# Kernel optimization log

Hardware: AMD Instinct MI355X
Metric: run time of the kernel (lower is better)

The kernel has to match this reference:

```python
import jax, jax.numpy as jnp
import numpy as np
from jax import lax

D_MODEL = 1024
STATE_DIM = 32
GROUPS = 8
GROUP_DIM = D_MODEL // GROUPS
DT_MIN = 0.001
DT_MAX = 0.1
EPS = 1e-6


def setup_inputs() -> dict:
    key = jax.random.key(0)
    ks = jax.random.split(key, 6)
    B, T = 4, 4096
    u = jax.random.normal(ks[0], (B, T, D_MODEL), dtype=jnp.float32)
    state = jnp.zeros((B, GROUPS, STATE_DIM), dtype=jnp.float32)
    A_log = jax.random.normal(ks[1], (GROUPS, STATE_DIM), dtype=jnp.float32) * 0.02
    B_param = jax.random.normal(ks[2], (GROUPS, STATE_DIM, GROUP_DIM), dtype=jnp.float32) * 0.02
    C = jax.random.normal(ks[3], (GROUPS, GROUP_DIM, STATE_DIM), dtype=jnp.float32) * 0.02
    Dp = jnp.zeros((GROUPS, GROUP_DIM), dtype=jnp.float32)
    dt_logit = jnp.zeros((GROUPS,), dtype=jnp.float32)
    return {"u": u, "state": state, "A_log": A_log, "B_param": B_param,
            "C": C, "Dp": Dp, "dt_logit": dt_logit}


def reference(u, state, A_log, B_param, C, Dp, dt_logit):
    Bsz, T, Dm = u.shape
    A = -jax.nn.softplus(A_log)                                  # [G,N]
    dt = DT_MIN + (DT_MAX - DT_MIN) * jax.nn.sigmoid(dt_logit)   # [G]
    dt_g = dt[:, None]                                           # [G,1]
    Abar = jnp.exp(A * dt_g)                                     # [G,N]
    # (exp(A dt) - 1)/A, stable for small |A|
    frac = jnp.where(jnp.abs(A) > EPS, (Abar - 1.0) / A,
                     jnp.broadcast_to(dt_g, A.shape))            # [G,N]
    Bbar = frac[..., None] * B_param                             # [G,N,gd]

    u_g = u.reshape(Bsz, T, GROUPS, GROUP_DIM)                   # [B,T,G,gd]
    # precompute input injections for all timesteps, then scan the LTI recurrence
    Bu = jnp.einsum('btgi,gni->btgn', u_g, Bbar)                 # [B,T,G,N]
    Bu_t = jnp.moveaxis(Bu, 1, 0)                                # [T,B,G,N]

    def step(s, bu):
        s = s * Abar + bu                                        # [B,G,N]
        return s, s

    s_final, states = lax.scan(step, state, Bu_t)                # states: [T,B,G,N]
    Cs = jnp.einsum('tbgn,gdn->btgd', states, C)                 # [B,T,G,gd]
    y = (Cs + Dp * u_g).reshape(Bsz, T, Dm)                      # [B,T,D]
    return y, s_final
```

## Files before the change

### kernel.cpp

```cpp
#include <hip/hip_runtime.h>
#include <hip/hip_bf16.h>

#define DM 1024
#define SD 32
#define NG 8
#define GD 128
#define BS 4
#define TT 4096
#define CL 64
#define NC (TT/CL)

typedef __attribute__((ext_vector_type(8))) short short8;
typedef __attribute__((ext_vector_type(4))) float f32x4;

#define WS_POWA  0
#define WS_STL   65536
#define WS_CARRY (WS_STL + 8388608)
#define WS_PAL   (WS_CARRY + 262144)

__device__ __forceinline__ unsigned short f2bf(float f) {
  __hip_bfloat16 h = __float2bfloat16(f);
  return __builtin_bit_cast(unsigned short, h);
}
__device__ __forceinline__ float bf2f(unsigned short h) {
  return __uint_as_float(((unsigned)h) << 16);
}
__device__ __forceinline__ float softplus_f(float x) {
  return (x > 20.f) ? x : log1pf(expf(x));
}
__device__ __forceinline__ short8 pack8(float4 a, float4 b) {
  short8 h;
  h[0]=(short)f2bf(a.x); h[1]=(short)f2bf(a.y); h[2]=(short)f2bf(a.z); h[3]=(short)f2bf(a.w);
  h[4]=(short)f2bf(b.x); h[5]=(short)f2bf(b.y); h[6]=(short)f2bf(b.z); h[7]=(short)f2bf(b.w);
  return h;
}

__global__ __launch_bounds__(64) void ka_bu_scan(const float* __restrict__ u,
                                                 const float* __restrict__ A_log,
                                                 const float* __restrict__ B_param,
                                                 const float* __restrict__ dt_logit,
                                                 unsigned char* __restrict__ ws) {
  const int bx = blockIdx.x;
  const int c = bx & (NC - 1);
  const int g = (bx >> 6) & (NG - 1);
  const int b = bx >> 9;
  const int l = threadIdx.x;
  const int lr = l & 15, lh = l >> 4;

  const float dtg = 0.001f + 0.099f * (1.f / (1.f + expf(-dt_logit[g])));

  float fracv[2];
  #pragma unroll
  for (int nt = 0; nt < 2; ++nt) {
    int n = nt * 16 + lr;
    float A = -softplus_f(A_log[g * SD + n]);
    float a = expf(A * dtg);
    fracv[nt] = (fabsf(A) > 1e-6f) ? (a - 1.f) / A : dtg;
  }
  float a_scan;
  {
    float A = -softplus_f(A_log[g * SD + (l & 31)]);
    a_scan = expf(A * dtg);
  }

  const float* bp = B_param + (size_t)g * SD * GD;
  short8 bfr[4][2];
  #pragma unroll
  for (int kt = 0; kt < 4; ++kt)
    #pragma unroll
    for (int nt = 0; nt < 2; ++nt) {
      const float* p = bp + (size_t)(nt * 16 + lr) * GD + kt * 32 + lh * 8;
      float4 v0 = *(const float4*)p;
      float4 v1 = *(const float4*)(p + 4);
      float s = fracv[nt];
      v0.x*=s; v0.y*=s; v0.z*=s; v0.w*=s;
      v1.x*=s; v1.y*=s; v1.z*=s; v1.w*=s;
      bfr[kt][nt] = pack8(v0, v1);
    }

  const float* up = u + ((size_t)b * TT + (size_t)c * CL) * DM + g * GD;
  float4 ub[2][4][2];
  #pragma unroll
  for (int kt = 0; kt < 2; ++kt)
    #pragma unroll
    for (int m = 0; m < 4; ++m) {
      const float* p = up + (size_t)(m * 16 + lr) * DM + kt * 32 + lh * 8;
      ub[kt][m][0] = *(const float4*)p;
      ub[kt][m][1] = *(const float4*)(p + 4);
    }

  f32x4 acc[4][2];
  #pragma unroll
  for (int m = 0; m < 4; ++m)
    #pragma unroll
    for (int nt = 0; nt < 2; ++nt)
      #pragma unroll
      for (int j = 0; j < 4; ++j) acc[m][nt][j] = 0.f;

  #pragma unroll
  for (int kt = 0; kt < 4; ++kt) {
    short8 af[4];
    #pragma unroll
    for (int m = 0; m < 4; ++m)
      af[m] = pack8(ub[kt & 1][m][0], ub[kt & 1][m][1]);
    if (kt < 2) {
      #pragma unroll
      for (int m = 0; m < 4; ++m) {
        const float* p = up + (size_t)(m * 16 + lr) * DM + (kt + 2) * 32 + lh * 8;
        ub[kt & 1][m][0] = *(const float4*)p;
        ub[kt & 1][m][1] = *(const float4*)(p + 4);
      }
    }
    #pragma unroll
    for (int m = 0; m < 4; ++m)
      #pragma unroll
      for (int nt = 0; nt < 2; ++nt)
        acc[m][nt] = __builtin_amdgcn_mfma_f32_16x16x32_bf16(af[m], bfr[kt][nt], acc[m][nt], 0, 0, 0);
  }

  __shared__ __align__(16) float sBu[CL * 33];
  __shared__ __align__(16) unsigned short sSt[CL * SD];
  #pragma unroll
  for (int m = 0; m < 4; ++m)
    #pragma unroll
    for (int nt = 0; nt < 2; ++nt)
      #pragma unroll
      for (int j = 0; j < 4; ++j) {
        int t = m * 16 + lh * 4 + j;
        sBu[t * 33 + (nt * 16 + lr)] = acc[m][nt][j];
      }
  __syncthreads();

  float* carry = (float*)(ws + WS_CARRY);
  if (l < SD) {
    float s = 0.f;
    #pragma unroll
    for (int t = 0; t < CL; ++t) {
      s = fmaf(s, a_scan, sBu[t * 33 + l]);
      sSt[t * SD + l] = f2bf(s);
    }
    carry[((b * NG + g) * NC + c) * SD + l] = s;
  }
  __syncthreads();

  unsigned short* stg = (unsigned short*)(ws + WS_STL) + ((size_t)((b * NC + c) * NG + g)) * CL * SD;
  #pragma unroll
  for (int p = 0; p < 4; ++p) {
    int off = (p * 64 + l) * 8;
    *(short8*)(stg + off) = *(short8*)(sSt + off);
  }

  if (b == 0 && c == 0 && l < SD) {
    float* powA = (float*)(ws + WS_POWA);
    float* powAL = (float*)(ws + WS_PAL);
    float p = 1.f;
    #pragma unroll
    for (int t = 0; t < CL; ++t) {
      p *= a_scan;
      powA[(g * CL + t) * SD + l] = p;
    }
    float aL = p;
    float q = 1.f;
    #pragma unroll
    for (int j = 0; j < CL; ++j) {
      powAL[(g * CL + j) * SD + l] = q;
      q *= aL;
    }
  }
}

__global__ __launch_bounds__(128) void kb_y(const float* __restrict__ u,
                                            const float* __restrict__ state0,
                                            const float* __restrict__ C,
                                            const float* __restrict__ Dp,
                                            unsigned char* __restrict__ ws,
                                            float* __restrict__ y,
                                            float* __restrict__ sfin) {
  const int bx = blockIdx.x;
  const int c = bx & (NC - 1);
  const int g = (bx >> 6) & (NG - 1);
  const int b = bx >> 9;
  const int tid = threadIdx.x;
  const int w = tid >> 6;
  const int l = tid & 63;
  const int lr = l & 15, lh = l >> 4;
  const int n = l & 31;

  const float* powA = (const float*)(ws + WS_POWA) + g * CL * SD;
  const float* powAL = (const float*)(ws + WS_PAL) + g * CL * SD;
  const float* carry = (const float*)(ws + WS_CARRY) + (size_t)(b * NG + g) * NC * SD;
  const unsigned short* stg = (const unsigned short*)(ws + WS_STL) + ((size_t)((b * NC + c) * NG + g)) * CL * SD;

  __shared__ __align__(16) float sY[32 * 132];

  bool need_u;
  {
    float2 dpc = *(const float2*)(Dp + g * GD + l * 2);
    need_u = __ballot((dpc.x != 0.f) || (dpc.y != 0.f)) != 0ULL;
  }

  float p;
  {
    float a0 = 0.f, a1 = 0.f, a2 = 0.f, a3 = 0.f;
    int cc = 0;
    while (cc + 8 <= c) {
      float ca[8], wt[8];
      #pragma unroll
      for (int e = 0; e < 8; ++e) {
        ca[e] = carry[(cc + e) * SD + n];
        wt[e] = powAL[(c - 1 - cc - e) * SD + n];
      }
      a0 = fmaf(wt[0], ca[0], a0); a1 = fmaf(wt[1], ca[1], a1);
      a2 = fmaf(wt[2], ca[2], a2); a3 = fmaf(wt[3], ca[3], a3);
      a0 = fmaf(wt[4], ca[4], a0); a1 = fmaf(wt[5], ca[5], a1);
      a2 = fmaf(wt[6], ca[6], a2); a3 = fmaf(wt[7], ca[7], a3);
      cc += 8;
    }
    for (; cc < c; ++cc)
      a0 = fmaf(powAL[(c - 1 - cc) * SD + n], carry[cc * SD + n], a0);
    p = fmaf(state0[(b * NG + g) * SD + n], powAL[c * SD + n], (a0 + a1) + (a2 + a3));
  }
  if (w == 0 && c == NC - 1 && l < SD) {
    const float aL = powA[(CL - 1) * SD + l];
    sfin[(b * NG + g) * SD + l] = fmaf(p, aL, carry[(NC - 1) * SD + l]);
  }

  float pr[8];
  #pragma unroll
  for (int e = 0; e < 8; ++e) pr[e] = __shfl(p, lh * 8 + e);

  short8 sf[4];
  #pragma unroll
  for (int tt = 0; tt < 4; ++tt) {
    int t = tt * 16 + lr;
    short8 sl = *(const short8*)(stg + t * SD + lh * 8);
    const float* pw = powA + t * SD + lh * 8;
    float4 pw0 = *(const float4*)pw;
    float4 pw1 = *(const float4*)(pw + 4);
    short8 hh;
    hh[0] = (short)f2bf(bf2f((unsigned short)sl[0]) + pw0.x * pr[0]);
    hh[1] = (short)f2bf(bf2f((unsigned short)sl[1]) + pw0.y * pr[1]);
    hh[2] = (short)f2bf(bf2f((unsigned short)sl[2]) + pw0.z * pr[2]);
    hh[3] = (short)f2bf(bf2f((unsigned short)sl[3]) + pw0.w * pr[3]);
    hh[4] = (short)f2bf(bf2f((unsigned short)sl[4]) + pw1.x * pr[4]);
    hh[5] = (short)f2bf(bf2f((unsigned short)sl[5]) + pw1.y * pr[5]);
    hh[6] = (short)f2bf(bf2f((unsigned short)sl[6]) + pw1.z * pr[6]);
    hh[7] = (short)f2bf(bf2f((unsigned short)sl[7]) + pw1.w * pr[7]);
    sf[tt] = hh;
  }

  const float* cp = C + (size_t)g * GD * SD;
  const size_t rowbase = ((size_t)b * TT + (size_t)c * CL) * DM + g * GD;

  short8 cf[4];
  #pragma unroll
  for (int dd = 0; dd < 4; ++dd) {
    int d = (w * 4 + dd) * 16 + lr;
    const float* pp = cp + (size_t)d * SD + lh * 8;
    float4 v0 = *(const float4*)pp;
    float4 v1 = *(const float4*)(pp + 4);
    cf[dd] = pack8(v0, v1);
  }
  f32x4 acc[4][4];
  #pragma unroll
  for (int dd = 0; dd < 4; ++dd)
    #pragma unroll
    for (int tt = 0; tt < 4; ++tt) {
      f32x4 z;
      #pragma unroll
      for (int j = 0; j < 4; ++j) z[j] = 0.f;
      acc[dd][tt] = __builtin_amdgcn_mfma_f32_16x16x32_bf16(cf[dd], sf[tt], z, 0, 0, 0);
    }

  const int sd4 = (tid & 31) * 4;
  float4 dpv = *(const float4*)(Dp + g * GD + sd4);

  #pragma unroll
  for (int tp = 0; tp < 2; ++tp) {
    if (tp) __syncthreads();
    #pragma unroll
    for (int dd = 0; dd < 4; ++dd)
      #pragma unroll
      for (int q = 0; q < 2; ++q) {
        int tt = tp * 2 + q;
        int tl = q * 16 + lr;
        int d0 = (w * 4 + dd) * 16 + lh * 4;
        *(float4*)(sY + tl * 132 + d0) = (float4){acc[dd][tt][0], acc[dd][tt][1],
                                                  acc[dd][tt][2], acc[dd][tt][3]};
      }
    __syncthreads();
    #pragma unroll
    for (int r = 0; r < 8; ++r) {
      int tl = r * 4 + (tid >> 5);
      int t = tp * 32 + tl;
      float4 v = *(const float4*)(sY + tl * 132 + sd4);
      size_t off = rowbase + (size_t)t * DM + sd4;
      if (need_u) {
        float4 u4 = *(const float4*)(u + off);
        v.x += dpv.x * u4.x; v.y += dpv.y * u4.y;
        v.z += dpv.z * u4.z; v.w += dpv.w * u4.w;
      }
      *(float4*)(y + off) = v;
    }
  }
}

extern "C" void kernel_launch(void* const* d_in, const int* in_sizes, int n_in,
                              void* d_out, int out_size, void* d_ws, size_t ws_size,
                              hipStream_t stream) {
  const float* u       = (const float*)d_in[0];
  const float* state0  = (const float*)d_in[1];
  const float* A_log   = (const float*)d_in[2];
  const float* B_param = (const float*)d_in[3];
  const float* C       = (const float*)d_in[4];
  const float* Dp      = (const float*)d_in[5];
  const float* dtl     = (const float*)d_in[6];
  float* y = (float*)d_out;
  unsigned char* ws = (unsigned char*)d_ws;
  float* sfin = y + (size_t)BS * TT * DM;

  ka_bu_scan<<<dim3(BS * NG * NC), dim3(64), 0, stream>>>(u, A_log, B_param, dtl, ws);
  kb_y<<<dim3(BS * NG * NC), dim3(128), 0, stream>>>(u, state0, C, Dp, ws, y, sfin);
}
```

Before: 43.44 us.

## Process two chunks per block in kb_y with 256 threads

The output kernel now handles two consecutive time chunks per block, using 4 waves that each own 2 d-tiles instead of 2 waves with 4. The carry-prefix reduction runs once for the first chunk, and the second chunk's prefix comes from one extra FMA. This removes half of the serial O(c) carry sums and halves the C fragment loads per chunk. In exchange there are half as many blocks and extra barriers between the two chunk passes that share the sY buffer.

```diff
diff --git a/kernel.cpp b/kernel.cpp
--- a/kernel.cpp
+++ b/kernel.cpp
@@ -169,66 +169,16 @@
   }
 }
 
-__global__ __launch_bounds__(128) void kb_y(const float* __restrict__ u,
-                                            const float* __restrict__ state0,
-                                            const float* __restrict__ C,
-                                            const float* __restrict__ Dp,
-                                            unsigned char* __restrict__ ws,
-                                            float* __restrict__ y,
-                                            float* __restrict__ sfin) {
-  const int bx = blockIdx.x;
-  const int c = bx & (NC - 1);
-  const int g = (bx >> 6) & (NG - 1);
-  const int b = bx >> 9;
-  const int tid = threadIdx.x;
-  const int w = tid >> 6;
-  const int l = tid & 63;
-  const int lr = l & 15, lh = l >> 4;
-  const int n = l & 31;
-
-  const float* powA = (const float*)(ws + WS_POWA) + g * CL * SD;
-  const float* powAL = (const float*)(ws + WS_PAL) + g * CL * SD;
-  const float* carry = (const float*)(ws + WS_CARRY) + (size_t)(b * NG + g) * NC * SD;
-  const unsigned short* stg = (const unsigned short*)(ws + WS_STL) + ((size_t)((b * NC + c) * NG + g)) * CL * SD;
-
-  __shared__ __align__(16) float sY[32 * 132];
-
-  bool need_u;
-  {
-    float2 dpc = *(const float2*)(Dp + g * GD + l * 2);
-    need_u = __ballot((dpc.x != 0.f) || (dpc.y != 0.f)) != 0ULL;
-  }
-
-  float p;
-  {
-    float a0 = 0.f, a1 = 0.f, a2 = 0.f, a3 = 0.f;
-    int cc = 0;
-    while (cc + 8 <= c) {
-      float ca[8], wt[8];
-      #pragma unroll
-      for (int e = 0; e < 8; ++e) {
-        ca[e] = carry[(cc + e) * SD + n];
-        wt[e] = powAL[(c - 1 - cc - e) * SD + n];
-      }
-      a0 = fmaf(wt[0], ca[0], a0); a1 = fmaf(wt[1], ca[1], a1);
-      a2 = fmaf(wt[2], ca[2], a2); a3 = fmaf(wt[3], ca[3], a3);
-      a0 = fmaf(wt[4], ca[4], a0); a1 = fmaf(wt[5], ca[5], a1);
-      a2 = fmaf(wt[6], ca[6], a2); a3 = fmaf(wt[7], ca[7], a3);
-      cc += 8;
-    }
-    for (; cc < c; ++cc)
-      a0 = fmaf(powAL[(c - 1 - cc) * SD + n], carry[cc * SD + n], a0);
-    p = fmaf(state0[(b * NG + g) * SD + n], powAL[c * SD + n], (a0 + a1) + (a2 + a3));
-  }
-  if (w == 0 && c == NC - 1 && l < SD) {
-    const float aL = powA[(CL - 1) * SD + l];
-    sfin[(b * NG + g) * SD + l] = fmaf(p, aL, carry[(NC - 1) * SD + l]);
-  }
-
-  float pr[8];
-  #pragma unroll
-  for (int e = 0; e < 8; ++e) pr[e] = __shfl(p, lh * 8 + e);
-
+__device__ __forceinline__ void kb_chunk(const unsigned short* __restrict__ stg,
+                                         const float* __restrict__ powA,
+                                         const float (&pr)[8],
+                                         const short8 (&cf)[2],
+                                         float* __restrict__ sY,
+                                         const float* __restrict__ u,
+                                         float* __restrict__ y,
+                                         size_t rowbase,
+                                         float4 dpv, bool need_u,
+                                         int tid, int w, int lr, int lh) {
   short8 sf[4];
   #pragma unroll
   for (int tt = 0; tt < 4; ++tt) {
@@ -249,21 +199,9 @@
     sf[tt] = hh;
   }
 
-  const float* cp = C + (size_t)g * GD * SD;
-  const size_t rowbase = ((size_t)b * TT + (size_t)c * CL) * DM + g * GD;
-
-  short8 cf[4];
-  #pragma unroll
-  for (int dd = 0; dd < 4; ++dd) {
-    int d = (w * 4 + dd) * 16 + lr;
-    const float* pp = cp + (size_t)d * SD + lh * 8;
-    float4 v0 = *(const float4*)pp;
-    float4 v1 = *(const float4*)(pp + 4);
-    cf[dd] = pack8(v0, v1);
-  }
-  f32x4 acc[4][4];
-  #pragma unroll
-  for (int dd = 0; dd < 4; ++dd)
+  f32x4 acc[2][4];
+  #pragma unroll
+  for (int dd = 0; dd < 2; ++dd)
     #pragma unroll
     for (int tt = 0; tt < 4; ++tt) {
       f32x4 z;
@@ -273,25 +211,23 @@
     }
 
   const int sd4 = (tid & 31) * 4;
-  float4 dpv = *(const float4*)(Dp + g * GD + sd4);
-
   #pragma unroll
   for (int tp = 0; tp < 2; ++tp) {
-    if (tp) __syncthreads();
-    #pragma unroll
-    for (int dd = 0; dd < 4; ++dd)
+    __syncthreads();
+    #pragma unroll
+    for (int dd = 0; dd < 2; ++dd)
       #pragma unroll
       for (int q = 0; q < 2; ++q) {
         int tt = tp * 2 + q;
         int tl = q * 16 + lr;
-        int d0 = (w * 4 + dd) * 16 + lh * 4;
+        int d0 = (w * 2 + dd) * 16 + lh * 4;
         *(float4*)(sY + tl * 132 + d0) = (float4){acc[dd][tt][0], acc[dd][tt][1],
                                                   acc[dd][tt][2], acc[dd][tt][3]};
       }
     __syncthreads();
     #pragma unroll
-    for (int r = 0; r < 8; ++r) {
-      int tl = r * 4 + (tid >> 5);
+    for (int r = 0; r < 4; ++r) {
+      int tl = r * 8 + (tid >> 5);
       int t = tp * 32 + tl;
       float4 v = *(const float4*)(sY + tl * 132 + sd4);
       size_t off = rowbase + (size_t)t * DM + sd4;
@@ -303,6 +239,90 @@
       *(float4*)(y + off) = v;
     }
   }
+}
+
+__global__ __launch_bounds__(256) void kb_y(const float* __restrict__ u,
+                                            const float* __restrict__ state0,
+                                            const float* __restrict__ C,
+                                            const float* __restrict__ Dp,
+                                            unsigned char* __restrict__ ws,
+                                            float* __restrict__ y,
+                                            float* __restrict__ sfin) {
+  const int bx = blockIdx.x;
+  const int pc = bx & (NC / 2 - 1);
+  const int g = (bx >> 5) & (NG - 1);
+  const int b = bx >> 8;
+  const int c0 = pc * 2;
+  const int tid = threadIdx.x;
+  const int w = tid >> 6;
+  const int l = tid & 63;
+  const int lr = l & 15, lh = l >> 4;
+  const int n = l & 31;
+
+  const float* powA = (const float*)(ws + WS_POWA) + g * CL * SD;
+  const float* powAL = (const float*)(ws + WS_PAL) + g * CL * SD;
+  const float* carry = (const float*)(ws + WS_CARRY) + (size_t)(b * NG + g) * NC * SD;
+  const unsigned short* stg0 = (const unsigned short*)(ws + WS_STL) + ((size_t)((b * NC + c0) * NG + g)) * CL * SD;
+  const unsigned short* stg1 = stg0 + (size_t)NG * CL * SD;
+
+  __shared__ __align__(16) float sY[32 * 132];
+
+  bool need_u;
+  {
+    float2 dpc = *(const float2*)(Dp + g * GD + l * 2);
+    need_u = __ballot((dpc.x != 0.f) || (dpc.y != 0.f)) != 0ULL;
+  }
+
+  float p0;
+  {
+    float a0 = 0.f, a1 = 0.f, a2 = 0.f, a3 = 0.f;
+    int cc = 0;
+    while (cc + 8 <= c0) {
+      float ca[8], wt[8];
+      #pragma unroll
+      for (int e = 0; e < 8; ++e) {
+        ca[e] = carry[(cc + e) * SD + n];
+        wt[e] = powAL[(c0 - 1 - cc - e) * SD + n];
+      }
+      a0 = fmaf(wt[0], ca[0], a0); a1 = fmaf(wt[1], ca[1], a1);
+      a2 = fmaf(wt[2], ca[2], a2); a3 = fmaf(wt[3], ca[3], a3);
+      a0 = fmaf(wt[4], ca[4], a0); a1 = fmaf(wt[5], ca[5], a1);
+      a2 = fmaf(wt[6], ca[6], a2); a3 = fmaf(wt[7], ca[7], a3);
+      cc += 8;
+    }
+    for (; cc < c0; ++cc)
+      a0 = fmaf(powAL[(c0 - 1 - cc) * SD + n], carry[cc * SD + n], a0);
+    p0 = fmaf(state0[(b * NG + g) * SD + n], powAL[c0 * SD + n], (a0 + a1) + (a2 + a3));
+  }
+  const float aL = powA[(CL - 1) * SD + n];
+  const float p1 = fmaf(p0, aL, carry[c0 * SD + n]);
+  if (pc == NC / 2 - 1 && w == 0 && l < SD)
+    sfin[(b * NG + g) * SD + l] = fmaf(p1, aL, carry[(NC - 1) * SD + l]);
+
+  float pr0[8], pr1[8];
+  #pragma unroll
+  for (int e = 0; e < 8; ++e) {
+    pr0[e] = __shfl(p0, lh * 8 + e);
+    pr1[e] = __shfl(p1, lh * 8 + e);
+  }
+
+  const float* cp = C + (size_t)g * GD * SD;
+  short8 cf[2];
+  #pragma unroll
+  for (int dd = 0; dd < 2; ++dd) {
+    int d = (w * 2 + dd) * 16 + lr;
+    const float* pp = cp + (size_t)d * SD + lh * 8;
+    float4 v0 = *(const float4*)pp;
+    float4 v1 = *(const float4*)(pp + 4);
+    cf[dd] = pack8(v0, v1);
+  }
+
+  const int sd4 = (tid & 31) * 4;
+  float4 dpv = *(const float4*)(Dp + g * GD + sd4);
+  const size_t rowbase0 = ((size_t)b * TT + (size_t)c0 * CL) * DM + g * GD;
+
+  kb_chunk(stg0, powA, pr0, cf, sY, u, y, rowbase0, dpv, need_u, tid, w, lr, lh);
+  kb_chunk(stg1, powA, pr1, cf, sY, u, y, rowbase0 + (size_t)CL * DM, dpv, need_u, tid, w, lr, lh);
 }
 
 extern "C" void kernel_launch(void* const* d_in, const int* in_sizes, int n_in,
@@ -320,5 +340,5 @@
   float* sfin = y + (size_t)BS * TT * DM;
 
   ka_bu_scan<<<dim3(BS * NG * NC), dim3(64), 0, stream>>>(u, A_log, B_param, dtl, ws);
-  kb_y<<<dim3(BS * NG * NC), dim3(128), 0, stream>>>(u, state0, C, Dp, ws, y, sfin);
-}
+  kb_y<<<dim3(BS * NG * NC / 2), dim3(256), 0, stream>>>(u, state0, C, Dp, ws, y, sfin);
+}
```

Result: no change. 43.87 us (+1.0%).

## Split chunk scan across both half-waves and prefetch all u tiles upfront

Applied to the files above, without the earlier changes.

Each 64-step chunk scan was run by only 32 lanes sequentially. It is now split into two 32-step halves, one per half-wave, and the second half is corrected with the first half's final state times powers of A. All u loads are also issued up front into registers instead of being double-buffered, and launch_bounds asks for 2 waves per SIMD. This shortens the serial scan latency and exposes more memory parallelism, at the cost of higher register pressure and extra multiplies in the fix-up pass.

```diff
diff --git a/kernel.cpp b/kernel.cpp
--- a/kernel.cpp
+++ b/kernel.cpp
@@ -35,32 +35,45 @@
   return h;
 }
 
-__global__ __launch_bounds__(64) void ka_bu_scan(const float* __restrict__ u,
-                                                 const float* __restrict__ A_log,
-                                                 const float* __restrict__ B_param,
-                                                 const float* __restrict__ dt_logit,
-                                                 unsigned char* __restrict__ ws) {
+__global__ __launch_bounds__(64, 2) void ka_bu_scan(const float* __restrict__ u,
+                                                    const float* __restrict__ A_log,
+                                                    const float* __restrict__ B_param,
+                                                    const float* __restrict__ dt_logit,
+                                                    unsigned char* __restrict__ ws) {
   const int bx = blockIdx.x;
   const int c = bx & (NC - 1);
   const int g = (bx >> 6) & (NG - 1);
   const int b = bx >> 9;
   const int l = threadIdx.x;
   const int lr = l & 15, lh = l >> 4;
+  const int n = l & 31;
+  const int seg = l >> 5;
+
+  const float* up = u + ((size_t)b * TT + (size_t)c * CL) * DM + g * GD;
+  float4 ub[4][4][2];
+  #pragma unroll
+  for (int kt = 0; kt < 4; ++kt)
+    #pragma unroll
+    for (int m = 0; m < 4; ++m) {
+      const float* p = up + (size_t)(m * 16 + lr) * DM + kt * 32 + lh * 8;
+      ub[kt][m][0] = *(const float4*)p;
+      ub[kt][m][1] = *(const float4*)(p + 4);
+    }
 
   const float dtg = 0.001f + 0.099f * (1.f / (1.f + expf(-dt_logit[g])));
 
   float fracv[2];
   #pragma unroll
   for (int nt = 0; nt < 2; ++nt) {
-    int n = nt * 16 + lr;
-    float A = -softplus_f(A_log[g * SD + n]);
+    int np = nt * 16 + lr;
+    float A = -softplus_f(A_log[g * SD + np]);
     float a = expf(A * dtg);
     fracv[nt] = (fabsf(A) > 1e-6f) ? (a - 1.f) / A : dtg;
   }
-  float a_scan;
+  float a_n;
   {
-    float A = -softplus_f(A_log[g * SD + (l & 31)]);
-    a_scan = expf(A * dtg);
+    float A = -softplus_f(A_log[g * SD + n]);
+    a_n = expf(A * dtg);
   }
 
   const float* bp = B_param + (size_t)g * SD * GD;
@@ -78,17 +91,6 @@
       bfr[kt][nt] = pack8(v0, v1);
     }
 
-  const float* up = u + ((size_t)b * TT + (size_t)c * CL) * DM + g * GD;
-  float4 ub[2][4][2];
-  #pragma unroll
-  for (int kt = 0; kt < 2; ++kt)
-    #pragma unroll
-    for (int m = 0; m < 4; ++m) {
-      const float* p = up + (size_t)(m * 16 + lr) * DM + kt * 32 + lh * 8;
-      ub[kt][m][0] = *(const float4*)p;
-      ub[kt][m][1] = *(const float4*)(p + 4);
-    }
-
   f32x4 acc[4][2];
   #pragma unroll
   for (int m = 0; m < 4; ++m)
@@ -102,15 +104,7 @@
     short8 af[4];
     #pragma unroll
     for (int m = 0; m < 4; ++m)
-      af[m] = pack8(ub[kt & 1][m][0], ub[kt & 1][m][1]);
-    if (kt < 2) {
-      #pragma unroll
-      for (int m = 0; m < 4; ++m) {
-        const float* p = up + (size_t)(m * 16 + lr) * DM + (kt + 2) * 32 + lh * 8;
-        ub[kt & 1][m][0] = *(const float4*)p;
-        ub[kt & 1][m][1] = *(const float4*)(p + 4);
-      }
-    }
+      af[m] = pack8(ub[kt][m][0], ub[kt][m][1]);
     #pragma unroll
     for (int m = 0; m < 4; ++m)
       #pragma unroll
@@ -131,15 +125,27 @@
       }
   __syncthreads();
 
+  float sloc[32];
+  float s = 0.f;
+  #pragma unroll
+  for (int t = 0; t < 32; ++t) {
+    s = fmaf(s, a_n, sBu[(seg * 32 + t) * 33 + n]);
+    sloc[t] = s;
+  }
+  const float s31 = __shfl(s, n);
   float* carry = (float*)(ws + WS_CARRY);
-  if (l < SD) {
-    float s = 0.f;
-    #pragma unroll
-    for (int t = 0; t < CL; ++t) {
-      s = fmaf(s, a_scan, sBu[t * 33 + l]);
-      sSt[t * SD + l] = f2bf(s);
-    }
-    carry[((b * NG + g) * NC + c) * SD + l] = s;
+  {
+    float pw = 1.f;
+    float vlast = 0.f;
+    #pragma unroll
+    for (int t = 0; t < 32; ++t) {
+      pw *= a_n;
+      float v = seg ? fmaf(pw, s31, sloc[t]) : sloc[t];
+      sSt[(seg * 32 + t) * SD + n] = f2bf(v);
+      vlast = v;
+    }
+    if (seg)
+      carry[((b * NG + g) * NC + c) * SD + n] = vlast;
   }
   __syncthreads();
 
@@ -156,7 +162,7 @@
     float p = 1.f;
     #pragma unroll
     for (int t = 0; t < CL; ++t) {
-      p *= a_scan;
+      p *= a_n;
       powA[(g * CL + t) * SD + l] = p;
     }
     float aL = p;
```

After: 43.86 us. About the same (+1.0%).
